# Performance work log

Hardware: AMD Instinct MI355X
Metric: run time of the kernel (lower is better)

The kernel has to match this reference:

```python
import math
import jax, jax.numpy as jnp
import numpy as np

B, L, N, DM, H = 4, 12, 512, 64, 8
D = DM // H
FACTOR = 5  # args.spatial_factor


def setup_inputs() -> dict:
    key = jax.random.key(0)
    ks = jax.random.split(key, 6)
    s = 1.0 / math.sqrt(DM)
    return {
        "queries": jax.random.normal(ks[0], (B, L, N, DM), jnp.float32),
        "keys": jax.random.normal(ks[1], (B, L, N, DM), jnp.float32),
        "values": jax.random.normal(ks[2], (B, L, N, DM), jnp.float32),
        "Wq": jax.random.normal(ks[3], (DM, DM), jnp.float32) * s,
        "bq": jnp.zeros((DM,), jnp.float32),
        "Wk": jax.random.normal(ks[4], (DM, DM), jnp.float32) * s,
        "bk": jnp.zeros((DM,), jnp.float32),
        "Wv": jax.random.normal(ks[5], (DM, DM), jnp.float32) * s,
        "bv": jnp.zeros((DM,), jnp.float32),
    }


def reference(queries, keys, values, Wq, bq, Wk, bk, Wv, bv):
    # QKV projections (torch nn.Linear), then split heads and move to [B,H,N,L,D]
    q = jnp.transpose((queries @ Wq + bq).reshape(B, L, N, H, D), (0, 3, 2, 1, 4))
    k = jnp.transpose((keys @ Wk + bk).reshape(B, L, N, H, D), (0, 3, 2, 1, 4))
    v = jnp.transpose((values @ Wv + bv).reshape(B, L, N, H, D), (0, 3, 2, 1, 4))

    sample_k = min(FACTOR * int(np.ceil(np.log(N))), N)  # = n_top = effect_N

    # --- _prob_QK: random K sampling over the N (spatial) axis ---
    idx = jax.random.randint(jax.random.key(42), (N, sample_k), 0, N)  # [N, sk]
    K_sample = k[:, :, idx]                       # [B,H,N,sk,L,D] gather
    # Q.unsqueeze(-2) @ K_sample^T -> [B,H,N,L,sk], then transposed to [B,H,L,N,sk]
    qk_s = jnp.einsum('bhnld,bhnsld->bhlns', q, K_sample)
    M = qk_s.max(axis=-1) - qk_s.sum(axis=-1) / N  # sparsity measure [B,H,L,N]
    _, M_top = jax.lax.top_k(M, sample_k)          # [B,H,L,n_top]

    q_t = jnp.transpose(q, (0, 1, 3, 2, 4))        # [B,H,L,N,D]
    Q_red = jnp.take_along_axis(q_t, M_top[..., None], axis=3)  # [B,H,L,n_top,D]
    scores = jnp.einsum('bhltd,bhnld->bhltn', Q_red, k) / math.sqrt(D)

    # --- context: mean of V over nodes, overwritten at top queries ---
    attn = jax.nn.softmax(scores, axis=-1)                        # [B,H,L,n_top,N]
    attn_ret = jnp.einsum('bhltn,bhnld->bhltd', attn, v)          # [B,H,L,n_top,D]
    ctx = jnp.broadcast_to(v.mean(axis=2)[:, :, :, None, :], (B, H, L, N, D))
    bi = jnp.arange(B)[:, None, None, None]
    hi = jnp.arange(H)[None, :, None, None]
    li = jnp.arange(L)[None, None, :, None]
    ctx = ctx.at[bi, hi, li, M_top].set(attn_ret)                 # scatter-write

    out = jnp.transpose(ctx, (0, 2, 3, 1, 4)).reshape(B, L, N, DM)
    return out  # dropout p=0.0 -> identity
```

## Files before the change

### kernel.cpp

```cpp
#include <hip/hip_runtime.h>
#include <stdint.h>
#include <math.h>

#define BB 4
#define LL 12
#define NN 512
#define DMM 64
#define HH 8
#define DD 8
#define SK 35
#define IDX_TOTAL (NN*SK)
#define PADK 12

__device__ __forceinline__ void tf2x32(uint32_t k0, uint32_t k1, uint32_t x0, uint32_t x1,
                                       uint32_t& o0, uint32_t& o1) {
  const uint32_t ks2 = k0 ^ k1 ^ 0x1BD11BDAu;
  uint32_t a = x0 + k0, b = x1 + k1;
#define TF_R(r) { a += b; b = (b << (r)) | (b >> (32 - (r))); b ^= a; }
  TF_R(13) TF_R(15) TF_R(26) TF_R(6)
  a += k1;  b += ks2 + 1u;
  TF_R(17) TF_R(29) TF_R(16) TF_R(24)
  a += ks2; b += k0 + 2u;
  TF_R(13) TF_R(15) TF_R(26) TF_R(6)
  a += k0;  b += k1 + 3u;
  TF_R(17) TF_R(29) TF_R(16) TF_R(24)
  a += k1;  b += ks2 + 4u;
  TF_R(13) TF_R(15) TF_R(26) TF_R(6)
  a += ks2; b += k0 + 5u;
#undef TF_R
  o0 = a; o1 = b;
}

__global__ __launch_bounds__(256) void proj_idx_kernel(
    const float* __restrict__ Xq, const float* __restrict__ Xk, const float* __restrict__ Xv,
    const float* __restrict__ Wq_, const float* __restrict__ Wk_, const float* __restrict__ Wv_,
    const float* __restrict__ bq_, const float* __restrict__ bk_, const float* __restrict__ bv_,
    float* __restrict__ Oq, float* __restrict__ Ok, float* __restrict__ Ov,
    int* __restrict__ idxT) {
  const int tz = blockIdx.y;
  if (tz == 3) {
    int gid = blockIdx.x * 256 + threadIdx.x;
    if (gid < IDX_TOTAL) {
      int r = gid & (NN - 1);
      int s = gid >> 9;
      uint32_t ka, kb;
      tf2x32(0u, 42u, 0u, 1u, ka, kb);
      uint32_t b1, b2;
      tf2x32(ka, kb, 0u, (uint32_t)(r * SK + s), b1, b2);
      idxT[gid] = (int)((b1 ^ b2) & (uint32_t)(NN - 1));
    }
    return;
  }
  const float* X    = (tz == 0) ? Xq  : (tz == 1) ? Xk  : Xv;
  const float* W    = (tz == 0) ? Wq_ : (tz == 1) ? Wk_ : Wv_;
  const float* bias = (tz == 0) ? bq_ : (tz == 1) ? bk_ : bv_;
  float* O          = (tz == 0) ? Oq  : (tz == 1) ? Ok  : Ov;

  __shared__ __align__(16) float Ws[64][64];
  __shared__ __align__(16) float Xs[64][68];
  __shared__ float bs[64];

  const int tid = threadIdx.x;
  const size_t rowBase = (size_t)blockIdx.x * 64;
  const float* Xb = X + rowBase * 64;
  #pragma unroll
  for (int i = 0; i < 4; ++i) {
    int idx = tid + i*256;
    ((float4*)Ws)[idx] = ((const float4*)W)[idx];
    int r = idx >> 4, c = (idx & 15) << 2;
    *(float4*)&Xs[r][c] = ((const float4*)Xb)[idx];
  }
  if (tid < 64) bs[tid] = bias[tid];
  __syncthreads();

  const int hcol = tid & 7;
  const int rb   = tid >> 3;
  float4 bv0 = *(float4*)&bs[hcol*8];
  float4 bv1 = *(float4*)&bs[hcol*8+4];
  float acc[2][8];
  #pragma unroll
  for (int i = 0; i < 2; ++i) {
    acc[i][0]=bv0.x; acc[i][1]=bv0.y; acc[i][2]=bv0.z; acc[i][3]=bv0.w;
    acc[i][4]=bv1.x; acc[i][5]=bv1.y; acc[i][6]=bv1.z; acc[i][7]=bv1.w;
  }
  #pragma unroll 8
  for (int m = 0; m < 64; ++m) {
    float4 w0 = *(const float4*)&Ws[m][hcol*8];
    float4 w1 = *(const float4*)&Ws[m][hcol*8+4];
    float x0 = Xs[rb][m];
    float x1 = Xs[rb+32][m];
    acc[0][0]=fmaf(x0,w0.x,acc[0][0]); acc[0][1]=fmaf(x0,w0.y,acc[0][1]);
    acc[0][2]=fmaf(x0,w0.z,acc[0][2]); acc[0][3]=fmaf(x0,w0.w,acc[0][3]);
    acc[0][4]=fmaf(x0,w1.x,acc[0][4]); acc[0][5]=fmaf(x0,w1.y,acc[0][5]);
    acc[0][6]=fmaf(x0,w1.z,acc[0][6]); acc[0][7]=fmaf(x0,w1.w,acc[0][7]);
    acc[1][0]=fmaf(x1,w0.x,acc[1][0]); acc[1][1]=fmaf(x1,w0.y,acc[1][1]);
    acc[1][2]=fmaf(x1,w0.z,acc[1][2]); acc[1][3]=fmaf(x1,w0.w,acc[1][3]);
    acc[1][4]=fmaf(x1,w1.x,acc[1][4]); acc[1][5]=fmaf(x1,w1.y,acc[1][5]);
    acc[1][6]=fmaf(x1,w1.z,acc[1][6]); acc[1][7]=fmaf(x1,w1.w,acc[1][7]);
  }
  #pragma unroll
  for (int i = 0; i < 2; ++i) {
    size_t R = rowBase + rb + 32*i;
    int bI = (int)(R / (LL*NN));
    int lI = (int)((R / NN) % LL);
    int nI = (int)(R % NN);
    size_t off = ((((size_t)bI*HH + hcol)*LL + lI)*NN + nI)*DD;
    *(float4*)&O[off]     = make_float4(acc[i][0],acc[i][1],acc[i][2],acc[i][3]);
    *(float4*)&O[off + 4] = make_float4(acc[i][4],acc[i][5],acc[i][6],acc[i][7]);
  }
}

__global__ __launch_bounds__(512) void fused_kernel(
    const float* __restrict__ Qt, const float* __restrict__ Kt,
    const float* __restrict__ Vt, const int* __restrict__ idxT,
    float* __restrict__ out) {
  const int bid = blockIdx.x;
  const int l = bid % LL;
  const int h = (bid / LL) % HH;
  const int b = bid / (LL*HH);
  const int tid = threadIdx.x;
  const int wave = tid >> 6, lane = tid & 63;

  __shared__ __align__(16) float Ks[NN][PADK];
  __shared__ uint64_t keys[NN];
  __shared__ int sel[NN];
  __shared__ int topIdxL[SK + 1];
  __shared__ __align__(16) float attnOut[SK][8];
  __shared__ __align__(16) float redD[8][64][8];
  __shared__ __align__(16) float vm[8];

  const size_t slabOff = (size_t)bid * (NN*DD);

  {
    const float4* kg = (const float4*)(Kt + slabOff);
    float4 a = kg[tid*2], c = kg[tid*2+1];
    *(float4*)&Ks[tid][0] = a; *(float4*)&Ks[tid][4] = c;
  }
  const float4* qp = (const float4*)(Qt + slabOff + (size_t)tid*DD);
  float4 qa = qp[0], qb = qp[1];
  int jv[SK];
  const int* gi = idxT + tid;
  #pragma unroll
  for (int s = 0; s < SK; ++s) jv[s] = gi[s*NN];
  sel[tid] = -1;
  __syncthreads();

  {
    float mx = -INFINITY, sm = 0.f;
    #pragma unroll
    for (int s = 0; s < SK; ++s) {
      int j = jv[s];
      float4 c0 = *(const float4*)&Ks[j][0];
      float4 c1 = *(const float4*)&Ks[j][4];
      float dot = qa.x*c0.x + qa.y*c0.y + qa.z*c0.z + qa.w*c0.w
                + qb.x*c1.x + qb.y*c1.y + qb.z*c1.z + qb.w*c1.w;
      mx = fmaxf(mx, dot);
      sm += dot;
    }
    float m = mx - sm * (1.0f/NN);
    uint32_t u = __float_as_uint(m);
    uint32_t fk = (u & 0x80000000u) ? ~u : (u | 0x80000000u);
    keys[tid] = ((uint64_t)fk << 32) | (uint32_t)(NN - 1 - tid);
  }
  __syncthreads();

  {
    uint64_t my = keys[tid];
    int cnt = 0;
    #pragma unroll 16
    for (int j = 0; j < NN; ++j) cnt += (keys[j] > my) ? 1 : 0;
    if (cnt < SK) { topIdxL[cnt] = tid; sel[tid] = cnt; }
  }
  __syncthreads();

  const float4* kp = (const float4*)(Kt + slabOff);
  const float4* vp = (const float4*)(Vt + slabOff);

  if (wave == 0) {
    float a[8] = {0,0,0,0,0,0,0,0};
    #pragma unroll
    for (int j = 0; j < 8; ++j) {
      const float4* vr = vp + (size_t)(lane + 64*j)*2;
      float4 v0 = vr[0], v1 = vr[1];
      a[0]+=v0.x; a[1]+=v0.y; a[2]+=v0.z; a[3]+=v0.w;
      a[4]+=v1.x; a[5]+=v1.y; a[6]+=v1.z; a[7]+=v1.w;
    }
    *(float4*)&redD[0][lane][0] = make_float4(a[0],a[1],a[2],a[3]);
    *(float4*)&redD[0][lane][4] = make_float4(a[4],a[5],a[6],a[7]);
    const int d = lane & 7, g = lane >> 3;
    float s = 0.f;
    #pragma unroll
    for (int k = 0; k < 8; ++k) s += redD[0][g*8+k][d];
    s += __shfl_xor(s, 8); s += __shfl_xor(s, 16); s += __shfl_xor(s, 32);
    if (lane < 8) vm[lane] = s * (1.0f/NN);
  } else {
    const int base = (wave - 1) * 5;
    auto do_rows = [&](int t1, int t2, bool has2) {
      const int n1 = topIdxL[t1];
      const int n2 = has2 ? topIdxL[t2] : n1;
      const float4* q1p = (const float4*)(Qt + slabOff + (size_t)n1*DD);
      const float4* q2p = (const float4*)(Qt + slabOff + (size_t)n2*DD);
      float4 q1a = q1p[0], q1b = q1p[1];
      float4 q2a = q2p[0], q2b = q2p[1];
      float p1[8], p2[8];
      float mx1 = -INFINITY, mx2 = -INFINITY;
      #pragma unroll
      for (int j = 0; j < 8; ++j) {
        int key = lane + 64*j;
        float4 ca = kp[key*2], cb = kp[key*2+1];
        float s1 = q1a.x*ca.x + q1a.y*ca.y + q1a.z*ca.z + q1a.w*ca.w
                 + q1b.x*cb.x + q1b.y*cb.y + q1b.z*cb.z + q1b.w*cb.w;
        float s2 = q2a.x*ca.x + q2a.y*ca.y + q2a.z*ca.z + q2a.w*ca.w
                 + q2b.x*cb.x + q2b.y*cb.y + q2b.z*cb.z + q2b.w*cb.w;
        s1 *= 0.35355339059327373f;
        s2 *= 0.35355339059327373f;
        p1[j] = s1; p2[j] = s2;
        mx1 = fmaxf(mx1, s1); mx2 = fmaxf(mx2, s2);
      }
      #pragma unroll
      for (int off = 32; off >= 1; off >>= 1) {
        mx1 = fmaxf(mx1, __shfl_xor(mx1, off));
        mx2 = fmaxf(mx2, __shfl_xor(mx2, off));
      }
      float sum1 = 0.f, sum2 = 0.f;
      #pragma unroll
      for (int j = 0; j < 8; ++j) {
        p1[j] = __expf(p1[j] - mx1); sum1 += p1[j];
        p2[j] = __expf(p2[j] - mx2); sum2 += p2[j];
      }
      #pragma unroll
      for (int off = 32; off >= 1; off >>= 1) {
        sum1 += __shfl_xor(sum1, off);
        sum2 += __shfl_xor(sum2, off);
      }
      float a1[8] = {0,0,0,0,0,0,0,0}, a2[8] = {0,0,0,0,0,0,0,0};
      #pragma unroll
      for (int j = 0; j < 8; ++j) {
        int key = lane + 64*j;
        float4 va = vp[key*2], vb = vp[key*2+1];
        float w1 = p1[j], w2 = p2[j];
        a1[0]=fmaf(w1,va.x,a1[0]); a1[1]=fmaf(w1,va.y,a1[1]);
        a1[2]=fmaf(w1,va.z,a1[2]); a1[3]=fmaf(w1,va.w,a1[3]);
        a1[4]=fmaf(w1,vb.x,a1[4]); a1[5]=fmaf(w1,vb.y,a1[5]);
        a1[6]=fmaf(w1,vb.z,a1[6]); a1[7]=fmaf(w1,vb.w,a1[7]);
        a2[0]=fmaf(w2,va.x,a2[0]); a2[1]=fmaf(w2,va.y,a2[1]);
        a2[2]=fmaf(w2,va.z,a2[2]); a2[3]=fmaf(w2,va.w,a2[3]);
        a2[4]=fmaf(w2,vb.x,a2[4]); a2[5]=fmaf(w2,vb.y,a2[5]);
        a2[6]=fmaf(w2,vb.z,a2[6]); a2[7]=fmaf(w2,vb.w,a2[7]);
      }
      const int d = lane & 7, g = lane >> 3;
      {
        *(float4*)&redD[wave][lane][0] = make_float4(a1[0],a1[1],a1[2],a1[3]);
        *(float4*)&redD[wave][lane][4] = make_float4(a1[4],a1[5],a1[6],a1[7]);
        float s = 0.f;
        #pragma unroll
        for (int k = 0; k < 8; ++k) s += redD[wave][g*8+k][d];
        s += __shfl_xor(s, 8); s += __shfl_xor(s, 16); s += __shfl_xor(s, 32);
        if (lane < 8) attnOut[t1][lane] = s * (1.0f / sum1);
      }
      if (has2) {
        *(float4*)&redD[wave][lane][0] = make_float4(a2[0],a2[1],a2[2],a2[3]);
        *(float4*)&redD[wave][lane][4] = make_float4(a2[4],a2[5],a2[6],a2[7]);
        float s = 0.f;
        #pragma unroll
        for (int k = 0; k < 8; ++k) s += redD[wave][g*8+k][d];
        s += __shfl_xor(s, 8); s += __shfl_xor(s, 16); s += __shfl_xor(s, 32);
        if (lane < 8) attnOut[t2][lane] = s * (1.0f / sum2);
      }
    };
    do_rows(base, base + 1, true);
    do_rows(base + 2, base + 3, true);
    do_rows(base + 4, base + 4, false);
  }
  __syncthreads();

  {
    int t = sel[tid];
    float4 o0, o1;
    if (t >= 0) { o0 = *(const float4*)&attnOut[t][0]; o1 = *(const float4*)&attnOut[t][4]; }
    else        { o0 = *(const float4*)&vm[0];         o1 = *(const float4*)&vm[4]; }
    float* ob = out + ((size_t)(b*LL + l)*NN + tid)*DMM + h*DD;
    *(float4*)&ob[0] = o0;
    *(float4*)&ob[4] = o1;
  }
}

extern "C" void kernel_launch(void* const* d_in, const int* in_sizes, int n_in,
                              void* d_out, int out_size, void* d_ws, size_t ws_size,
                              hipStream_t stream) {
  const float* q  = (const float*)d_in[0];
  const float* k  = (const float*)d_in[1];
  const float* v  = (const float*)d_in[2];
  const float* Wq = (const float*)d_in[3];
  const float* bq = (const float*)d_in[4];
  const float* Wk = (const float*)d_in[5];
  const float* bk = (const float*)d_in[6];
  const float* Wv = (const float*)d_in[7];
  const float* bv = (const float*)d_in[8];
  float* out = (float*)d_out;

  const size_t slab = (size_t)BB*HH*LL*NN*DD;
  float* qT = (float*)d_ws;
  float* kT = qT + slab;
  float* vT = kT + slab;
  int*   idxT = (int*)(vT + slab);

  proj_idx_kernel<<<dim3((BB*LL*NN)/64, 4), 256, 0, stream>>>(
      q, k, v, Wq, Wk, Wv, bq, bk, bv, qT, kT, vT, idxT);
  fused_kernel<<<BB*HH*LL, 512, 0, stream>>>(qT, kT, vT, idxT, out);
}
```

Measured before the change: 59.94 us.

## Split sparsity-measure computation into separate kernel and use 32-bit rank keys

Moves the sampled Q·K sparsity-measure computation out of the fused attention kernel into a new kernel launched over twice as many blocks, which writes 32-bit sortable keys to workspace. The fused kernel then reads those keys and ranks them with vectorized 32-bit comparisons and an explicit index tie-break, replacing the 64-bit packed keys. This frees shared memory in the fused kernel and spreads the sampling work across more blocks. In exchange it adds a kernel launch and a global round-trip for the keys.

Result: slower. 81.55 us (+36.1%).

```diff
diff --git a/kernel.cpp b/kernel.cpp
--- a/kernel.cpp
+++ b/kernel.cpp
@@ -29,6 +29,11 @@
   a += ks2; b += k0 + 5u;
 #undef TF_R
   o0 = a; o1 = b;
+}
+
+__device__ __forceinline__ uint32_t fkey(float m) {
+  uint32_t u = __float_as_uint(m);
+  return (u & 0x80000000u) ? ~u : (u | 0x80000000u);
 }
 
 __global__ __launch_bounds__(256) void proj_idx_kernel(
@@ -110,9 +115,48 @@
   }
 }
 
+__global__ __launch_bounds__(256) void mkeys_kernel(
+    const float* __restrict__ Qt, const float* __restrict__ Kt,
+    const int* __restrict__ idxT, uint32_t* __restrict__ keysW) {
+  const int gb = blockIdx.x;
+  const int bid = gb >> 1, half = gb & 1;
+  const int tid = threadIdx.x;
+  __shared__ __align__(16) float Ks[NN][PADK];
+  const size_t slabOff = (size_t)bid * (NN*DD);
+
+  const float4* kg = (const float4*)(Kt + slabOff);
+  #pragma unroll
+  for (int i = 0; i < 2; ++i) {
+    int r = tid + i*256;
+    float4 a = kg[r*2], c = kg[r*2+1];
+    *(float4*)&Ks[r][0] = a; *(float4*)&Ks[r][4] = c;
+  }
+  const int row = half*256 + tid;
+  const float4* qp = (const float4*)(Qt + slabOff + (size_t)row*DD);
+  float4 qa = qp[0], qb = qp[1];
+  int jv[SK];
+  const int* gi = idxT + row;
+  #pragma unroll
+  for (int s = 0; s < SK; ++s) jv[s] = gi[s*NN];
+  __syncthreads();
+
+  float mx = -INFINITY, sm = 0.f;
+  #pragma unroll
+  for (int s = 0; s < SK; ++s) {
+    int j = jv[s];
+    float4 c0 = *(const float4*)&Ks[j][0];
+    float4 c1 = *(const float4*)&Ks[j][4];
+    float dot = qa.x*c0.x + qa.y*c0.y + qa.z*c0.z + qa.w*c0.w
+              + qb.x*c1.x + qb.y*c1.y + qb.z*c1.z + qb.w*c1.w;
+    mx = fmaxf(mx, dot);
+    sm += dot;
+  }
+  keysW[bid*NN + row] = fkey(mx - sm * (1.0f/NN));
+}
+
 __global__ __launch_bounds__(512) void fused_kernel(
     const float* __restrict__ Qt, const float* __restrict__ Kt,
-    const float* __restrict__ Vt, const int* __restrict__ idxT,
+    const float* __restrict__ Vt, const uint32_t* __restrict__ keysW,
     float* __restrict__ out) {
   const int bid = blockIdx.x;
   const int l = bid % LL;
@@ -121,8 +165,7 @@
   const int tid = threadIdx.x;
   const int wave = tid >> 6, lane = tid & 63;
 
-  __shared__ __align__(16) float Ks[NN][PADK];
-  __shared__ uint64_t keys[NN];
+  __shared__ __align__(16) uint32_t keys32[NN];
   __shared__ int sel[NN];
   __shared__ int topIdxL[SK + 1];
   __shared__ __align__(16) float attnOut[SK][8];
@@ -131,44 +174,23 @@
 
   const size_t slabOff = (size_t)bid * (NN*DD);
 
+  const uint32_t my = keysW[bid*NN + tid];
+  keys32[tid] = my;
+  sel[tid] = -1;
+  __syncthreads();
+
   {
-    const float4* kg = (const float4*)(Kt + slabOff);
-    float4 a = kg[tid*2], c = kg[tid*2+1];
-    *(float4*)&Ks[tid][0] = a; *(float4*)&Ks[tid][4] = c;
-  }
-  const float4* qp = (const float4*)(Qt + slabOff + (size_t)tid*DD);
-  float4 qa = qp[0], qb = qp[1];
-  int jv[SK];
-  const int* gi = idxT + tid;
-  #pragma unroll
-  for (int s = 0; s < SK; ++s) jv[s] = gi[s*NN];
-  sel[tid] = -1;
-  __syncthreads();
-
-  {
-    float mx = -INFINITY, sm = 0.f;
-    #pragma unroll
-    for (int s = 0; s < SK; ++s) {
-      int j = jv[s];
-      float4 c0 = *(const float4*)&Ks[j][0];
-      float4 c1 = *(const float4*)&Ks[j][4];
-      float dot = qa.x*c0.x + qa.y*c0.y + qa.z*c0.z + qa.w*c0.w
-                + qb.x*c1.x + qb.y*c1.y + qb.z*c1.z + qb.w*c1.w;
-      mx = fmaxf(mx, dot);
-      sm += dot;
+    const uint4* kq = (const uint4*)keys32;
+    int cnt = 0;
+    #pragma unroll 8
+    for (int jb = 0; jb < NN/4; ++jb) {
+      uint4 kv = kq[jb];
+      int j0 = jb*4;
+      cnt += (kv.x > my || (kv.x == my && j0     < tid)) ? 1 : 0;
+      cnt += (kv.y > my || (kv.y == my && j0 + 1 < tid)) ? 1 : 0;
+      cnt += (kv.z > my || (kv.z == my && j0 + 2 < tid)) ? 1 : 0;
+      cnt += (kv.w > my || (kv.w == my && j0 + 3 < tid)) ? 1 : 0;
     }
-    float m = mx - sm * (1.0f/NN);
-    uint32_t u = __float_as_uint(m);
-    uint32_t fk = (u & 0x80000000u) ? ~u : (u | 0x80000000u);
-    keys[tid] = ((uint64_t)fk << 32) | (uint32_t)(NN - 1 - tid);
-  }
-  __syncthreads();
-
-  {
-    uint64_t my = keys[tid];
-    int cnt = 0;
-    #pragma unroll 16
-    for (int j = 0; j < NN; ++j) cnt += (keys[j] > my) ? 1 : 0;
     if (cnt < SK) { topIdxL[cnt] = tid; sel[tid] = cnt; }
   }
   __syncthreads();
@@ -304,8 +326,10 @@
   float* kT = qT + slab;
   float* vT = kT + slab;
   int*   idxT = (int*)(vT + slab);
+  uint32_t* keysW = (uint32_t*)(idxT + IDX_TOTAL);
 
   proj_idx_kernel<<<dim3((BB*LL*NN)/64, 4), 256, 0, stream>>>(
       q, k, v, Wq, Wk, Wv, bq, bk, bv, qT, kT, vT, idxT);
-  fused_kernel<<<BB*HH*LL, 512, 0, stream>>>(qT, kT, vT, idxT, out);
-}
+  mkeys_kernel<<<BB*HH*LL*2, 256, 0, stream>>>(qT, kT, idxT, keysW);
+  fused_kernel<<<BB*HH*LL, 512, 0, stream>>>(qT, kT, vT, keysW, out);
+}
```
